# Performance work log

Measured on AMD Instinct MI355X. Metric: run time of the kernel, lower is better.

Reference implementation:

```python
import jax, jax.numpy as jnp
import numpy as np

N, E, G = 50000, 1600000, 512
IN, HID, PROJ = 128, 128, 256


def setup_inputs() -> dict:
    key = jax.random.key(0)
    ks = jax.random.split(key, 20)
    s = 0.05
    return {
        'x1': jax.random.normal(ks[0], (N, IN), jnp.float32),
        'edge_index1': jax.random.randint(ks[1], (2, E), 0, N),
        'batch1': jnp.sort(jax.random.randint(ks[2], (N,), 0, G)),
        'x2': jax.random.normal(ks[3], (N, IN), jnp.float32),
        'edge_index2': jax.random.randint(ks[4], (2, E), 0, N),
        'batch2': jnp.sort(jax.random.randint(ks[5], (N,), 0, G)),
        'W1': jax.random.normal(ks[6], (IN, HID), jnp.float32) * s,
        'b1': jnp.zeros((HID,), jnp.float32),
        'W2': jax.random.normal(ks[7], (HID, HID), jnp.float32) * s,
        'b2': jnp.zeros((HID,), jnp.float32),
        'W3': jax.random.normal(ks[8], (HID, HID), jnp.float32) * s,
        'b3': jnp.zeros((HID,), jnp.float32),
        'Wp1': jax.random.normal(ks[9], (HID, PROJ), jnp.float32) * s,
        'bp1': jnp.zeros((PROJ,), jnp.float32),
        'gamma1': jnp.ones((PROJ,), jnp.float32),
        'beta1': jnp.zeros((PROJ,), jnp.float32),
        'Wp2': jax.random.normal(ks[10], (PROJ, PROJ), jnp.float32) * s,
        'bp2': jnp.zeros((PROJ,), jnp.float32),
        'gamma2': jnp.ones((PROJ,), jnp.float32),
        'beta2': jnp.zeros((PROJ,), jnp.float32),
        'Wq1': jax.random.normal(ks[11], (PROJ, PROJ // 2), jnp.float32) * s,
        'bq1': jnp.zeros((PROJ // 2,), jnp.float32),
        'Wq2': jax.random.normal(ks[12], (PROJ // 2, PROJ), jnp.float32) * s,
        'bq2': jnp.zeros((PROJ,), jnp.float32),
    }


def _gcn_conv(x, src, dst, W, b):
    # PyG GCNConv: add self-loops, symmetric norm, gather -> scatter-add
    n = x.shape[0]
    h = x @ W                                   # [n, out]
    loop = jnp.arange(n)
    s = jnp.concatenate([src, loop])
    d = jnp.concatenate([dst, loop])
    deg = jax.ops.segment_sum(jnp.ones(s.shape[0], h.dtype), d, num_segments=n)
    dinv = jnp.where(deg > 0, 1.0 / jnp.sqrt(deg), 0.0)
    norm = (dinv[s] * dinv[d])[:, None]         # [E+n, 1]
    out = jax.ops.segment_sum(h[s] * norm, d, num_segments=n)
    return out + b


def _encode(x, edge_index, batch, W1, b1, W2, b2, W3, b3):
    src, dst = edge_index[0], edge_index[1]
    h = jax.nn.relu(_gcn_conv(x, src, dst, W1, b1))
    h = jax.nn.relu(_gcn_conv(h, src, dst, W2, b2)) + h
    h = jax.nn.relu(_gcn_conv(h, src, dst, W3, b3)) + h
    # global mean pool over graph ids
    s = jax.ops.segment_sum(h, batch, num_segments=G)
    cnt = jax.ops.segment_sum(jnp.ones(h.shape[0], h.dtype), batch, num_segments=G)
    return s / jnp.maximum(cnt, 1.0)[:, None]


def _batchnorm(x, gamma, beta):
    m = x.mean(axis=0)
    v = x.var(axis=0)  # biased, matches torch BN normalization
    return gamma * (x - m) / jnp.sqrt(v + 1e-5) + beta


def _projector(h, Wp1, bp1, g1, be1, Wp2, bp2, g2, be2):
    z = jax.nn.relu(_batchnorm(h @ Wp1 + bp1, g1, be1))
    return _batchnorm(z @ Wp2 + bp2, g2, be2)


def _predictor(z, Wq1, bq1, Wq2, bq2):
    return jax.nn.relu(z @ Wq1 + bq1) @ Wq2 + bq2


def reference(x1, edge_index1, batch1, x2, edge_index2, batch2,
              W1, b1, W2, b2, W3, b3,
              Wp1, bp1, gamma1, beta1, Wp2, bp2, gamma2, beta2,
              Wq1, bq1, Wq2, bq2):
    h1 = _encode(x1, edge_index1, batch1, W1, b1, W2, b2, W3, b3)
    h2 = _encode(x2, edge_index2, batch2, W1, b1, W2, b2, W3, b3)
    z1 = _projector(h1, Wp1, bp1, gamma1, beta1, Wp2, bp2, gamma2, beta2)
    z2 = _projector(h2, Wp1, bp1, gamma1, beta1, Wp2, bp2, gamma2, beta2)
    p1 = _predictor(z1, Wq1, bq1, Wq2, bq2)
    p2 = _predictor(z2, Wq1, bq1, Wq2, bq2)
    return (p1, p2, z1, z2)
```

## Files before the change

### kernel.cpp

```cpp
#include <hip/hip_runtime.h>
#include <hip/hip_bf16.h>

#define NN     50000
#define NN2    100000
#define NEDGE  1600000
#define NE2    3200000
#define NG     512
#define FIN    128
#define FHID   128
#define FPROJ  256

#define BSH    9
#define BSZ    512
#define NBUCK  98
#define NBUCK2 196
#define EPB    8192
#define NABLK  196
#define NABLK2 392
#define NHIST2 (NBUCK2*NABLK2)

typedef __attribute__((ext_vector_type(8))) short short8;
typedef __attribute__((ext_vector_type(4))) float f32x4;

static __device__ __forceinline__ short f2bf(float f) {
    union { float f; unsigned u; } x; x.f = f;
    unsigned r = (x.u + 0x7FFFu + ((x.u >> 16) & 1u)) >> 16;
    return (short)(r & 0xFFFFu);
}
static __device__ __forceinline__ float bf2f(unsigned short u) {
    union { unsigned u; float f; } x; x.u = ((unsigned)u) << 16;
    return x.f;
}
static __device__ __forceinline__ float bflo(unsigned u) {
    union { unsigned u; float f; } x; x.u = u << 16; return x.f;
}
static __device__ __forceinline__ float bfhi(unsigned u) {
    union { unsigned u; float f; } x; x.u = u & 0xFFFF0000u; return x.f;
}
static __device__ __forceinline__ unsigned packbf(float a, float b) {
    return (unsigned)(unsigned short)f2bf(a) | ((unsigned)(unsigned short)f2bf(b) << 16);
}


__global__ __launch_bounds__(1024) void k_bhist(const int* __restrict__ dst0,
                                                const int* __restrict__ dst1,
                                                int* __restrict__ histG,
                                                unsigned short* __restrict__ lrank) {
    __shared__ int h[NBUCK2];
    for (int j = threadIdx.x; j < NBUCK2; j += 1024) h[j] = 0;
    __syncthreads();
    int b = blockIdx.x;
    int g = b / NABLK, blk = b % NABLK;
    const int* dst = g ? dst1 : dst0;
    int base = blk * EPB;
    int gb = g * NBUCK;
    for (int t = threadIdx.x; t < EPB; t += 1024) {
        int i = base + t;
        if (i < NEDGE)
            lrank[(size_t)g * NEDGE + i] =
                (unsigned short)atomicAdd(&h[gb + (dst[i] >> BSH)], 1);
    }
    __syncthreads();
    for (int j = threadIdx.x; j < NBUCK2; j += 1024)
        histG[(size_t)j * NABLK2 + b] = h[j];
}

__global__ void s_scan256(const int* __restrict__ in, int* __restrict__ out,
                          int* __restrict__ bsum, int n) {
    __shared__ int s[256];
    int i = blockIdx.x * 256 + threadIdx.x;
    int v = (i < n) ? in[i] : 0;
    s[threadIdx.x] = v;
    for (int o = 1; o < 256; o <<= 1) {
        __syncthreads();
        int t = (threadIdx.x >= o) ? s[threadIdx.x - o] : 0;
        __syncthreads();
        s[threadIdx.x] += t;
    }
    __syncthreads();
    if (i < n) out[i] = s[threadIdx.x] - v;
    if (threadIdx.x == 255 && bsum) bsum[blockIdx.x] = s[255];
}

__global__ void s_add(int* __restrict__ out, const int* __restrict__ bs, int n) {
    int i = blockIdx.x * 256 + threadIdx.x;
    if (i < n) out[i] += bs[blockIdx.x];
}

__global__ __launch_bounds__(1024) void k_part(const int* __restrict__ src0,
                                               const int* __restrict__ dst0,
                                               const int* __restrict__ src1,
                                               const int* __restrict__ dst1,
                                               const unsigned short* __restrict__ lrank,
                                               const int* __restrict__ histS,
                                               unsigned* __restrict__ pedge) {
    int b = blockIdx.x;
    int g = b / NABLK, blk = b % NABLK;
    const int* src = g ? src1 : src0;
    const int* dst = g ? dst1 : dst0;
    int base = blk * EPB;
    int gb = g * NBUCK;
    for (int t = threadIdx.x; t < EPB; t += 1024) {
        int i = base + t;
        if (i < NEDGE) {
            int d = dst[i];
            int pos = histS[(size_t)(gb + (d >> BSH)) * NABLK2 + b]
                      + (int)lrank[(size_t)g * NEDGE + i];
            pedge[pos] = (unsigned)src[i] | ((unsigned)(d & (BSZ - 1)) << 16);
        }
    }
}

__global__ __launch_bounds__(256) void k_csr(const unsigned* __restrict__ pedge,
                                             const int* __restrict__ histS,
                                             int* __restrict__ csroff,
                                             unsigned short* __restrict__ csrc,
                                             float* __restrict__ dinv) {
    __shared__ int cnt[BSZ], off[BSZ], cur[BSZ];
    int k = blockIdx.x;
    int g = k / NBUCK;
    int nl0 = (k - g * NBUCK) * BSZ;
    int beg = histS[(size_t)k * NABLK2];
    int end = (k == NBUCK2 - 1) ? NE2 : histS[(size_t)(k + 1) * NABLK2];
    for (int t = threadIdx.x; t < BSZ; t += 256) { cnt[t] = 0; cur[t] = 0; }
    __syncthreads();
    for (int e = beg + threadIdx.x; e < end; e += 256)
        atomicAdd(&cnt[(pedge[e] >> 16) & (BSZ - 1)], 1);
    __syncthreads();
    if (threadIdx.x == 0) {
        int s = 0;
        for (int j = 0; j < BSZ; ++j) { off[j] = s; s += cnt[j]; }
    }
    __syncthreads();
    for (int e = beg + threadIdx.x; e < end; e += 256) {
        unsigned v = pedge[e];
        int j = (v >> 16) & (BSZ - 1);
        int r = atomicAdd(&cur[j], 1);
        csrc[beg + off[j] + r] = (unsigned short)(v & 0xFFFFu);
    }
    __syncthreads();
    for (int t = threadIdx.x; t < BSZ; t += 256) {
        int nl = nl0 + t;
        if (nl < NN) {
            int gn = g * NN + nl;
            csroff[gn] = beg + off[t];
            dinv[gn] = 1.0f / sqrtf((float)(cnt[t] + 1));
        }
    }
    if (k == NBUCK2 - 1 && threadIdx.x == 0) csroff[NN2] = NE2;
}


__global__ void k_prepw(const float* __restrict__ W0, const float* __restrict__ W1,
                        const float* __restrict__ W2, short* __restrict__ Wf) {
    int b = blockIdx.x;
    int l = b >> 5; b &= 31;
    const float* W = (l == 0) ? W0 : (l == 1) ? W1 : W2;
    int nt = b >> 2, kt = b & 3;
    int lane = threadIdx.x;
    int n = nt * 16 + (lane & 15);
    int kbase = kt * 32 + (lane >> 4) * 8;
    short8 v;
#pragma unroll
    for (int j = 0; j < 8; ++j) v[j] = f2bf(W[(kbase + j) * FHID + n]);
    *(short8*)(Wf + (size_t)l * 16384 + (size_t)((nt * 4 + kt) * 64 + lane) * 8) = v;
}

__global__ __launch_bounds__(256) void k_gemm(const float* __restrict__ x1,
                                              const float* __restrict__ x2,
                                              const unsigned short* __restrict__ Abf,
                                              const short* __restrict__ Wf,
                                              const float* __restrict__ dinv,
                                              unsigned short* __restrict__ hp) {
    int lane = threadIdx.x & 63;
    int wv = threadIdx.x >> 6;
    int quad = lane >> 4;
    int rowbase = blockIdx.x * 64 + wv * 16;
    int arow = rowbase + (lane & 15);
    if (arow >= NN2) arow = NN2 - 1;

    f32x4 acc[8];
#pragma unroll
    for (int i = 0; i < 8; ++i) acc[i] = (f32x4){0.f, 0.f, 0.f, 0.f};

#pragma unroll
    for (int kt = 0; kt < 4; ++kt) {
        short8 af;
        if (Abf) {
            af = *(const short8*)(Abf + (size_t)arow * FIN + kt * 32 + quad * 8);
        } else {
            const float* ap = (arow < NN ? x1 + (size_t)arow * FIN
                                         : x2 + (size_t)(arow - NN) * FIN)
                              + kt * 32 + quad * 8;
            float4 a0 = *(const float4*)ap;
            float4 a1 = *(const float4*)(ap + 4);
            af[0] = f2bf(a0.x); af[1] = f2bf(a0.y); af[2] = f2bf(a0.z); af[3] = f2bf(a0.w);
            af[4] = f2bf(a1.x); af[5] = f2bf(a1.y); af[6] = f2bf(a1.z); af[7] = f2bf(a1.w);
        }
#pragma unroll
        for (int nt = 0; nt < 8; ++nt) {
            short8 bf = *(const short8*)(Wf + (size_t)((nt * 4 + kt) * 64 + lane) * 8);
            acc[nt] = __builtin_amdgcn_mfma_f32_16x16x32_bf16(af, bf, acc[nt], 0, 0, 0);
        }
    }
    float4 dv = *(const float4*)(dinv + rowbase + quad * 4);
    float dvv[4] = {dv.x, dv.y, dv.z, dv.w};
    int col = lane & 15;
#pragma unroll
    for (int r = 0; r < 4; ++r) {
        int orow = rowbase + quad * 4 + r;
        if (orow < NN2) {
#pragma unroll
            for (int nt = 0; nt < 8; ++nt)
                hp[(size_t)orow * FHID + nt * 16 + col] =
                    (unsigned short)f2bf(acc[nt][r] * dvv[r]);
        }
    }
}


__global__ __launch_bounds__(256) void k_agg(const uint2* __restrict__ hp,
                                             const int* __restrict__ off,
                                             const unsigned short* __restrict__ csrc,
                                             const float* __restrict__ dinv,
                                             const float* __restrict__ bias,
                                             const unsigned short* __restrict__ resid,
                                             unsigned short* __restrict__ hout) {
    int tid = threadIdx.x;
    int l2 = tid & 31;
    int node = blockIdx.x * 8 + (tid >> 5);
    int beg = off[node], end = off[node + 1];

    uint2 sv = hp[(size_t)node * 32 + l2];
    float a0 = bflo(sv.x), a1 = bfhi(sv.x), a2 = bflo(sv.y), a3 = bfhi(sv.y);

    int e = beg;
    for (; e + 16 <= end; e += 16) {
        int s[16];
#pragma unroll
        for (int j = 0; j < 16; ++j) s[j] = (int)csrc[e + j];
        uint2 v[16];
#pragma unroll
        for (int j = 0; j < 16; ++j) v[j] = hp[(size_t)s[j] * 32 + l2];
#pragma unroll
        for (int j = 0; j < 16; ++j) {
            a0 += bflo(v[j].x); a1 += bfhi(v[j].x);
            a2 += bflo(v[j].y); a3 += bfhi(v[j].y);
        }
    }
    for (; e + 4 <= end; e += 4) {
        int s[4];
#pragma unroll
        for (int j = 0; j < 4; ++j) s[j] = (int)csrc[e + j];
        uint2 v[4];
#pragma unroll
        for (int j = 0; j < 4; ++j) v[j] = hp[(size_t)s[j] * 32 + l2];
#pragma unroll
        for (int j = 0; j < 4; ++j) {
            a0 += bflo(v[j].x); a1 += bfhi(v[j].x);
            a2 += bflo(v[j].y); a3 += bfhi(v[j].y);
        }
    }
    for (; e < end; ++e) {
        uint2 v = hp[(size_t)csrc[e] * 32 + l2];
        a0 += bflo(v.x); a1 += bfhi(v.x);
        a2 += bflo(v.y); a3 += bfhi(v.y);
    }
    float dv = dinv[node];
    float4 b = ((const float4*)bias)[l2];
    float o0 = fmaxf(a0 * dv + b.x, 0.f);
    float o1 = fmaxf(a1 * dv + b.y, 0.f);
    float o2 = fmaxf(a2 * dv + b.z, 0.f);
    float o3 = fmaxf(a3 * dv + b.w, 0.f);
    if (resid) {
        uint2 rv = ((const uint2*)resid)[(size_t)node * 32 + l2];
        o0 += bflo(rv.x); o1 += bfhi(rv.x);
        o2 += bflo(rv.y); o3 += bfhi(rv.y);
    }
    uint2 ov;
    ov.x = packbf(o0, o1);
    ov.y = packbf(o2, o3);
    ((uint2*)hout)[(size_t)node * 32 + l2] = ov;
}


__global__ void k_starts(const int* __restrict__ b0, const int* __restrict__ b1,
                         int* __restrict__ starts) {
    int blk = blockIdx.x;
    int g = blk / NABLK;
    int i = (blk - g * NABLK) * 256 + threadIdx.x;
    if (i >= NN) return;
    const int* batch = g ? b1 : b0;
    int* st = starts + g * (NG + 1);
    int b = batch[i];
    if (i == 0) {
        for (int q = 0; q <= b; ++q) st[q] = 0;
    } else {
        int p = batch[i - 1];
        for (int q = p + 1; q <= b; ++q) st[q] = i;
    }
    if (i == NN - 1) {
        for (int q = b + 1; q <= NG; ++q) st[q] = NN;
    }
}

__global__ void k_pool(const unsigned short* __restrict__ h, const int* __restrict__ starts,
                       float* __restrict__ pooled) {
    int b = blockIdx.x;
    int g = b >> 9, lg = b & 511;
    int c = threadIdx.x;
    const int* st = starts + g * (NG + 1);
    const unsigned short* hb = h + (size_t)g * NN * FHID;
    int beg = st[lg], end = st[lg + 1];
    float s = 0.f;
    for (int i = beg; i < end; ++i) s += bf2f(hb[(size_t)i * FHID + c]);
    int cnt = end - beg;
    pooled[(size_t)b * FHID + c] = s / (float)(cnt > 0 ? cnt : 1);
}


__global__ void k_mlp(const float* __restrict__ A, const float* __restrict__ W,
                      const float* __restrict__ bias, float* __restrict__ out,
                      int K, int Nc, int act,
                      float* __restrict__ statsOut,
                      const float* __restrict__ statsIn,
                      const float* __restrict__ gIn, const float* __restrict__ beIn) {
    __shared__ float As[8 * 256];
    __shared__ float scl[256], shf[256];
    int n = threadIdx.x;
    int r0 = blockIdx.x * 8;
    int g = blockIdx.x >> 6;
    if (statsIn && n < K) {
        const float* si = statsIn + g * 512;
        float m = si[n] * (1.f / 512.f);
        float var = si[K + n] * (1.f / 512.f) - m * m;
        float inv = 1.0f / sqrtf(var + 1e-5f);
        float s = gIn[n] * inv;
        scl[n] = s;
        shf[n] = beIn[n] - m * s;
    }
    __syncthreads();
    for (int idx = n; idx < 8 * K; idx += blockDim.x) {
        float v = A[(size_t)r0 * K + idx];
        if (statsIn) {
            int k = idx & (K - 1);
            v = fmaxf(v * scl[k] + shf[k], 0.f);
        }
        As[idx] = v;
    }
    __syncthreads();
    float bb = bias[n];
    float acc[8];
#pragma unroll
    for (int r = 0; r < 8; ++r) acc[r] = bb;
    for (int k = 0; k < K; ++k) {
        float w = W[(size_t)k * Nc + n];
#pragma unroll
        for (int r = 0; r < 8; ++r) acc[r] = fmaf(As[r * K + k], w, acc[r]);
    }
    if (statsOut) {
        float s = 0.f, q = 0.f;
#pragma unroll
        for (int r = 0; r < 8; ++r) { s += acc[r]; q += acc[r] * acc[r]; }
        atomicAdd(&statsOut[g * 512 + n], s);
        atomicAdd(&statsOut[g * 512 + Nc + n], q);
    }
#pragma unroll
    for (int r = 0; r < 8; ++r) {
        float v = acc[r];
        if (act) v = fmaxf(v, 0.f);
        out[(size_t)(r0 + r) * Nc + n] = v;
    }
}

__global__ void k_bnapply(const float* __restrict__ X, const float* __restrict__ stats,
                          const float* __restrict__ gamma, const float* __restrict__ beta,
                          float* __restrict__ out, int Nc, int act) {
    int i = blockIdx.x * 256 + threadIdx.x;
    if (i >= 1024 * Nc) return;
    int c = i % Nc;
    int g = i / (512 * Nc);
    const float* st = stats + g * 512;
    float m = st[c] * (1.f / 512.f);
    float var = st[Nc + c] * (1.f / 512.f) - m * m;
    float inv = 1.0f / sqrtf(var + 1e-5f);
    float v = gamma[c] * (X[i] - m) * inv + beta[c];
    if (act) v = fmaxf(v, 0.f);
    out[i] = v;
}


extern "C" void kernel_launch(void* const* d_in, const int* in_sizes, int n_in,
                              void* d_out, int out_size, void* d_ws, size_t ws_size,
                              hipStream_t stream) {
    const float* x1 = (const float*)d_in[0];
    const float* x2 = (const float*)d_in[3];
    const int*   ei[2]    = {(const int*)d_in[1], (const int*)d_in[4]};
    const int*   batch[2] = {(const int*)d_in[2], (const int*)d_in[5]};
    const float* W[3]  = {(const float*)d_in[6], (const float*)d_in[8], (const float*)d_in[10]};
    const float* bb[3] = {(const float*)d_in[7], (const float*)d_in[9], (const float*)d_in[11]};
    const float* Wp1 = (const float*)d_in[12]; const float* bp1 = (const float*)d_in[13];
    const float* g1  = (const float*)d_in[14]; const float* be1 = (const float*)d_in[15];
    const float* Wp2 = (const float*)d_in[16]; const float* bp2 = (const float*)d_in[17];
    const float* g2  = (const float*)d_in[18]; const float* be2 = (const float*)d_in[19];
    const float* Wq1 = (const float*)d_in[20]; const float* bq1 = (const float*)d_in[21];
    const float* Wq2 = (const float*)d_in[22]; const float* bq2 = (const float*)d_in[23];

    char* ws = (char*)d_ws;
    size_t off = 0;
    auto alloc = [&](size_t bytes) -> void* {
        void* p = ws + off;
        off += (bytes + 255) & ~(size_t)255;
        return p;
    };
    unsigned short* h_cur  = (unsigned short*)alloc((size_t)NN2 * FHID * 2);
    unsigned short* hp     = (unsigned short*)alloc((size_t)NN2 * FHID * 2);
    unsigned short* csrc   = (unsigned short*)alloc((size_t)NE2 * 2);
    int*            csroff = (int*)alloc((size_t)(NN2 + 1) * 4);
    unsigned short* lrank  = (unsigned short*)alloc((size_t)NE2 * 2);
    unsigned*       pedge  = (unsigned*)alloc((size_t)NE2 * 4);
    int*            histG  = (int*)alloc((size_t)NHIST2 * 4);
    int*            histS  = (int*)alloc((size_t)NHIST2 * 4);
    int*            bsum1  = (int*)alloc(512 * 4);
    int*            bsum1s = (int*)alloc(512 * 4);
    int*            bsum2  = (int*)alloc(256 * 4);
    int*            bsum2s = (int*)alloc(256 * 4);
    float*          dinv   = (float*)alloc((size_t)100352 * 4);
    int*            starts = (int*)alloc(2 * (NG + 1) * 4);
    float*          pooled = (float*)alloc((size_t)2 * NG * FHID * 4);
    short*          Wf     = (short*)alloc((size_t)3 * 16384 * 2);
    float*          t1     = (float*)alloc((size_t)1024 * 256 * 4);
    float*          t2     = (float*)alloc((size_t)1024 * 256 * 4);
    float*          t3     = (float*)alloc((size_t)1024 * 128 * 4);
    float*          stats  = (float*)alloc(2048 * 4);

    const int* src0 = ei[0];           const int* dst0 = ei[0] + NEDGE;
    const int* src1 = ei[1];           const int* dst1 = ei[1] + NEDGE;

    k_prepw<<<96, 64, 0, stream>>>(W[0], W[1], W[2], Wf);

    const int nsb1 = (NHIST2 + 255) / 256;
    const int nsb2 = (nsb1 + 255) / 256;
    k_bhist<<<NABLK2, 1024, 0, stream>>>(dst0, dst1, histG, lrank);
    s_scan256<<<nsb1, 256, 0, stream>>>(histG, histS, bsum1, NHIST2);
    s_scan256<<<nsb2, 256, 0, stream>>>(bsum1, bsum1s, bsum2, nsb1);
    s_scan256<<<1, 256, 0, stream>>>(bsum2, bsum2s, nullptr, nsb2);
    s_add<<<nsb2, 256, 0, stream>>>(bsum1s, bsum2s, nsb1);
    s_add<<<nsb1, 256, 0, stream>>>(histS, bsum1s, NHIST2);
    k_part<<<NABLK2, 1024, 0, stream>>>(src0, dst0, src1, dst1, lrank, histS, pedge);
    k_csr<<<NBUCK2, 256, 0, stream>>>(pedge, histS, csroff, csrc, dinv);

    for (int l = 0; l < 3; ++l) {
        const unsigned short* Abf = (l == 0) ? nullptr : h_cur;
        k_gemm<<<1564, 256, 0, stream>>>(x1, x2, Abf, Wf + (size_t)l * 16384, dinv, hp);
        for (int g = 0; g < 2; ++g) {
            size_t nb = (size_t)g * NN;
            const unsigned short* resid = (l == 0) ? nullptr : h_cur + nb * FHID;
            k_agg<<<6250, 256, 0, stream>>>((const uint2*)(hp + nb * FHID),
                                            csroff + nb, csrc, dinv + nb,
                                            bb[l], resid, h_cur + nb * FHID);
        }
    }
    k_starts<<<NABLK2, 256, 0, stream>>>(batch[0], batch[1], starts);
    k_pool<<<1024, 128, 0, stream>>>(h_cur, starts, pooled);

    float* outp = (float*)d_out;
    float* p_out = outp;
    float* z_out = outp + (size_t)2 * NG * FPROJ;
    float* st1 = stats, *st2 = stats + 1024;
    hipMemsetAsync(stats, 0, 2048 * 4, stream);
    k_mlp<<<128, 256, 0, stream>>>(pooled, Wp1, bp1, t1,
                                   128, 256, 0, st1, nullptr, nullptr, nullptr);
    k_mlp<<<128, 256, 0, stream>>>(t1, Wp2, bp2, t2,
                                   256, 256, 0, st2, st1, g1, be1);
    k_bnapply<<<1024, 256, 0, stream>>>(t2, st2, g2, be2, z_out, 256, 0);
    k_mlp<<<128, 128, 0, stream>>>(z_out, Wq1, bq1, t3,
                                   256, 128, 1, nullptr, nullptr, nullptr, nullptr);
    k_mlp<<<128, 256, 0, stream>>>(t3, Wq2, bq2, p_out,
                                   128, 256, 0, nullptr, nullptr, nullptr, nullptr);
}
```

Before: 753.1 us.

## Cut launch count: single-block scan, merged graph aggregation, fused pool setup

Replaces the five-kernel hierarchical scan with one 1024-thread block that scans the whole histogram in per-thread chunks. Both graphs are now aggregated in one k_agg launch, the k_starts kernel is replaced by binary searches on the sorted batch inside k_pool, and zeroing the stats buffer moves into k_pool in place of the memset. The aim is to cut kernel launches and the gaps between them. In exchange, the scan runs on a single CU with strided, uncoalesced per-thread loops over about 77K entries, which may be slow.

Measured after the change: 809.0 us. 7.4% more time.

```diff
diff --git a/kernel.cpp b/kernel.cpp
--- a/kernel.cpp
+++ b/kernel.cpp
@@ -65,26 +65,24 @@
         histG[(size_t)j * NABLK2 + b] = h[j];
 }
 
-__global__ void s_scan256(const int* __restrict__ in, int* __restrict__ out,
-                          int* __restrict__ bsum, int n) {
-    __shared__ int s[256];
-    int i = blockIdx.x * 256 + threadIdx.x;
-    int v = (i < n) ? in[i] : 0;
-    s[threadIdx.x] = v;
-    for (int o = 1; o < 256; o <<= 1) {
+__global__ __launch_bounds__(1024) void s_scan_all(const int* __restrict__ in,
+                                                   int* __restrict__ out, int n) {
+    __shared__ int s[1024];
+    int chunk = (n + 1023) / 1024;
+    int b = threadIdx.x * chunk;
+    int e = b + chunk; if (e > n) e = n;
+    int sum = 0;
+    for (int i = b; i < e; ++i) sum += in[i];
+    s[threadIdx.x] = sum;
+    for (int o = 1; o < 1024; o <<= 1) {
         __syncthreads();
         int t = (threadIdx.x >= o) ? s[threadIdx.x - o] : 0;
         __syncthreads();
         s[threadIdx.x] += t;
     }
     __syncthreads();
-    if (i < n) out[i] = s[threadIdx.x] - v;
-    if (threadIdx.x == 255 && bsum) bsum[blockIdx.x] = s[255];
-}
-
-__global__ void s_add(int* __restrict__ out, const int* __restrict__ bs, int n) {
-    int i = blockIdx.x * 256 + threadIdx.x;
-    if (i < n) out[i] += bs[blockIdx.x];
+    int run = s[threadIdx.x] - sum;
+    for (int i = b; i < e; ++i) { int v = in[i]; out[i] = run; run += v; }
 }
 
 __global__ __launch_bounds__(1024) void k_part(const int* __restrict__ src0,
@@ -228,10 +226,15 @@
                                              unsigned short* __restrict__ hout) {
     int tid = threadIdx.x;
     int l2 = tid & 31;
-    int node = blockIdx.x * 8 + (tid >> 5);
-    int beg = off[node], end = off[node + 1];
-
-    uint2 sv = hp[(size_t)node * 32 + l2];
+    int g = blockIdx.x / 6250;
+    int lb = blockIdx.x - g * 6250;
+    int node = lb * 8 + (tid >> 5);
+    size_t nb = (size_t)g * NN;
+    const uint2* hpg = hp + nb * 32;
+    int gn = (int)nb + node;
+    int beg = off[gn], end = off[gn + 1];
+
+    uint2 sv = hpg[(size_t)node * 32 + l2];
     float a0 = bflo(sv.x), a1 = bfhi(sv.x), a2 = bflo(sv.y), a3 = bfhi(sv.y);
 
     int e = beg;
@@ -241,7 +244,7 @@
         for (int j = 0; j < 16; ++j) s[j] = (int)csrc[e + j];
         uint2 v[16];
 #pragma unroll
-        for (int j = 0; j < 16; ++j) v[j] = hp[(size_t)s[j] * 32 + l2];
+        for (int j = 0; j < 16; ++j) v[j] = hpg[(size_t)s[j] * 32 + l2];
 #pragma unroll
         for (int j = 0; j < 16; ++j) {
             a0 += bflo(v[j].x); a1 += bfhi(v[j].x);
@@ -254,7 +257,7 @@
         for (int j = 0; j < 4; ++j) s[j] = (int)csrc[e + j];
         uint2 v[4];
 #pragma unroll
-        for (int j = 0; j < 4; ++j) v[j] = hp[(size_t)s[j] * 32 + l2];
+        for (int j = 0; j < 4; ++j) v[j] = hpg[(size_t)s[j] * 32 + l2];
 #pragma unroll
         for (int j = 0; j < 4; ++j) {
             a0 += bflo(v[j].x); a1 += bfhi(v[j].x);
@@ -262,56 +265,47 @@
         }
     }
     for (; e < end; ++e) {
-        uint2 v = hp[(size_t)csrc[e] * 32 + l2];
+        uint2 v = hpg[(size_t)csrc[e] * 32 + l2];
         a0 += bflo(v.x); a1 += bfhi(v.x);
         a2 += bflo(v.y); a3 += bfhi(v.y);
     }
-    float dv = dinv[node];
+    float dv = dinv[gn];
     float4 b = ((const float4*)bias)[l2];
     float o0 = fmaxf(a0 * dv + b.x, 0.f);
     float o1 = fmaxf(a1 * dv + b.y, 0.f);
     float o2 = fmaxf(a2 * dv + b.z, 0.f);
     float o3 = fmaxf(a3 * dv + b.w, 0.f);
     if (resid) {
-        uint2 rv = ((const uint2*)resid)[(size_t)node * 32 + l2];
+        uint2 rv = ((const uint2*)resid)[(size_t)gn * 32 + l2];
         o0 += bflo(rv.x); o1 += bfhi(rv.x);
         o2 += bflo(rv.y); o3 += bfhi(rv.y);
     }
     uint2 ov;
     ov.x = packbf(o0, o1);
     ov.y = packbf(o2, o3);
-    ((uint2*)hout)[(size_t)node * 32 + l2] = ov;
-}
-
-
-__global__ void k_starts(const int* __restrict__ b0, const int* __restrict__ b1,
-                         int* __restrict__ starts) {
-    int blk = blockIdx.x;
-    int g = blk / NABLK;
-    int i = (blk - g * NABLK) * 256 + threadIdx.x;
-    if (i >= NN) return;
-    const int* batch = g ? b1 : b0;
-    int* st = starts + g * (NG + 1);
-    int b = batch[i];
-    if (i == 0) {
-        for (int q = 0; q <= b; ++q) st[q] = 0;
-    } else {
-        int p = batch[i - 1];
-        for (int q = p + 1; q <= b; ++q) st[q] = i;
-    }
-    if (i == NN - 1) {
-        for (int q = b + 1; q <= NG; ++q) st[q] = NN;
-    }
-}
-
-__global__ void k_pool(const unsigned short* __restrict__ h, const int* __restrict__ starts,
-                       float* __restrict__ pooled) {
+    ((uint2*)hout)[(size_t)gn * 32 + l2] = ov;
+}
+
+
+static __device__ __forceinline__ int lbound(const int* __restrict__ a, int key) {
+    int lo = 0, hi = NN;
+    while (lo < hi) { int mid = (lo + hi) >> 1; if (a[mid] < key) lo = mid + 1; else hi = mid; }
+    return lo;
+}
+
+__global__ void k_pool(const unsigned short* __restrict__ h,
+                       const int* __restrict__ b0, const int* __restrict__ b1,
+                       float* __restrict__ pooled, float* __restrict__ stats) {
     int b = blockIdx.x;
     int g = b >> 9, lg = b & 511;
     int c = threadIdx.x;
-    const int* st = starts + g * (NG + 1);
+    if (b == 0) {
+        for (int i = c; i < 2048; i += 128) stats[i] = 0.f;
+    }
+    const int* batch = g ? b1 : b0;
+    int beg = lbound(batch, lg);
+    int end = lbound(batch, lg + 1);
     const unsigned short* hb = h + (size_t)g * NN * FHID;
-    int beg = st[lg], end = st[lg + 1];
     float s = 0.f;
     for (int i = beg; i < end; ++i) s += bf2f(hb[(size_t)i * FHID + c]);
     int cnt = end - beg;
@@ -421,12 +415,7 @@
     unsigned*       pedge  = (unsigned*)alloc((size_t)NE2 * 4);
     int*            histG  = (int*)alloc((size_t)NHIST2 * 4);
     int*            histS  = (int*)alloc((size_t)NHIST2 * 4);
-    int*            bsum1  = (int*)alloc(512 * 4);
-    int*            bsum1s = (int*)alloc(512 * 4);
-    int*            bsum2  = (int*)alloc(256 * 4);
-    int*            bsum2s = (int*)alloc(256 * 4);
     float*          dinv   = (float*)alloc((size_t)100352 * 4);
-    int*            starts = (int*)alloc(2 * (NG + 1) * 4);
     float*          pooled = (float*)alloc((size_t)2 * NG * FHID * 4);
     short*          Wf     = (short*)alloc((size_t)3 * 16384 * 2);
     float*          t1     = (float*)alloc((size_t)1024 * 256 * 4);
@@ -439,36 +428,24 @@
 
     k_prepw<<<96, 64, 0, stream>>>(W[0], W[1], W[2], Wf);
 
-    const int nsb1 = (NHIST2 + 255) / 256;
-    const int nsb2 = (nsb1 + 255) / 256;
     k_bhist<<<NABLK2, 1024, 0, stream>>>(dst0, dst1, histG, lrank);
-    s_scan256<<<nsb1, 256, 0, stream>>>(histG, histS, bsum1, NHIST2);
-    s_scan256<<<nsb2, 256, 0, stream>>>(bsum1, bsum1s, bsum2, nsb1);
-    s_scan256<<<1, 256, 0, stream>>>(bsum2, bsum2s, nullptr, nsb2);
-    s_add<<<nsb2, 256, 0, stream>>>(bsum1s, bsum2s, nsb1);
-    s_add<<<nsb1, 256, 0, stream>>>(histS, bsum1s, NHIST2);
+    s_scan_all<<<1, 1024, 0, stream>>>(histG, histS, NHIST2);
     k_part<<<NABLK2, 1024, 0, stream>>>(src0, dst0, src1, dst1, lrank, histS, pedge);
     k_csr<<<NBUCK2, 256, 0, stream>>>(pedge, histS, csroff, csrc, dinv);
 
     for (int l = 0; l < 3; ++l) {
         const unsigned short* Abf = (l == 0) ? nullptr : h_cur;
+        const unsigned short* resid = (l == 0) ? nullptr : h_cur;
         k_gemm<<<1564, 256, 0, stream>>>(x1, x2, Abf, Wf + (size_t)l * 16384, dinv, hp);
-        for (int g = 0; g < 2; ++g) {
-            size_t nb = (size_t)g * NN;
-            const unsigned short* resid = (l == 0) ? nullptr : h_cur + nb * FHID;
-            k_agg<<<6250, 256, 0, stream>>>((const uint2*)(hp + nb * FHID),
-                                            csroff + nb, csrc, dinv + nb,
-                                            bb[l], resid, h_cur + nb * FHID);
-        }
-    }
-    k_starts<<<NABLK2, 256, 0, stream>>>(batch[0], batch[1], starts);
-    k_pool<<<1024, 128, 0, stream>>>(h_cur, starts, pooled);
+        k_agg<<<12500, 256, 0, stream>>>((const uint2*)hp, csroff, csrc, dinv,
+                                         bb[l], resid, h_cur);
+    }
+    k_pool<<<1024, 128, 0, stream>>>(h_cur, batch[0], batch[1], pooled, stats);
 
     float* outp = (float*)d_out;
     float* p_out = outp;
     float* z_out = outp + (size_t)2 * NG * FPROJ;
     float* st1 = stats, *st2 = stats + 1024;
-    hipMemsetAsync(stats, 0, 2048 * 4, stream);
     k_mlp<<<128, 256, 0, stream>>>(pooled, Wp1, bp1, t1,
                                    128, 256, 0, st1, nullptr, nullptr, nullptr);
     k_mlp<<<128, 256, 0, stream>>>(t1, Wp2, bp2, t2,
```
